# Kernel tuning notes

Hardware: AMD Instinct MI355X
Metric: run time of the kernel (lower is better)

Reference implementation:

```python
import jax, jax.numpy as jnp
import numpy as np

H = 1.0  # RBF bandwidth (init kwarg h)


def setup_inputs() -> dict:
    key = jax.random.key(0)
    k1, k2 = jax.random.split(key)
    x = jax.random.normal(k1, (8192, 512), dtype=jnp.float32)
    x1 = jax.random.normal(k2, (8192, 512), dtype=jnp.float32)
    return {"x": x, "x1": x1}


def reference(x, x1):
    # exp(-||x_i - x1_j||^2 / h), computed via the GEMM trick to avoid the
    # O(N*M*D) broadcast intermediate the original torch code materializes.
    x_sq = jnp.sum(x * x, axis=-1, keepdims=True)          # [N, 1]
    x1_sq = jnp.sum(x1 * x1, axis=-1)                       # [M]
    cross = jnp.einsum('nd,md->nm', x, x1)                  # [N, M]
    d = jnp.maximum(x_sq + x1_sq[None, :] - 2.0 * cross, 0.0)
    return jnp.exp(-d / H)
```

## Files before the change

### kernel.cpp

```cpp
#include <hip/hip_runtime.h>
#include <stdint.h>
#include <stddef.h>


#define NROWS 8192
#define DIMK  512
#define BM    128
#define BN    128
#define BK    32
#define KTILES (DIMK / BK)

typedef __bf16 bf16x8 __attribute__((ext_vector_type(8)));
typedef float  f32x4  __attribute__((ext_vector_type(4)));

#define AS1 __attribute__((address_space(1)))
#define AS3 __attribute__((address_space(3)))

__device__ __forceinline__ uint32_t f2bf(float f) {
    uint32_t u = __float_as_uint(f);
    return (u + 0x7FFFu + ((u >> 16) & 1u)) >> 16;
}

__global__ __launch_bounds__(256) void precast_full(
    const float* __restrict__ x, const float* __restrict__ x1,
    uint16_t* __restrict__ xb, uint16_t* __restrict__ x1b,
    float* __restrict__ xsq, float* __restrict__ x1sq)
{
    const int row = blockIdx.x;
    const float* src;
    uint16_t* dstb;
    float* dsts;
    if (blockIdx.y == 0) { src = x  + (size_t)row * DIMK; dstb = xb  + (size_t)row * DIMK; dsts = xsq  + row; }
    else                 { src = x1 + (size_t)row * DIMK; dstb = x1b + (size_t)row * DIMK; dsts = x1sq + row; }
    const int t = threadIdx.x;
    float2 v = ((const float2*)src)[t];
    float s = v.x * v.x + v.y * v.y;
    ((uint32_t*)dstb)[t] = f2bf(v.x) | (f2bf(v.y) << 16);
    #pragma unroll
    for (int off = 32; off > 0; off >>= 1) s += __shfl_down(s, off);
    __shared__ float red[4];
    if ((t & 63) == 0) red[t >> 6] = s;
    __syncthreads();
    if (t == 0) *dsts = red[0] + red[1] + red[2] + red[3];
}

__global__ __launch_bounds__(256) void norms_only(
    const float* __restrict__ x, const float* __restrict__ x1,
    float* __restrict__ xsq, float* __restrict__ x1sq)
{
    const int row = blockIdx.x;
    const float* src = (blockIdx.y == 0) ? x + (size_t)row * DIMK : x1 + (size_t)row * DIMK;
    float* dsts      = (blockIdx.y == 0) ? xsq + row : x1sq + row;
    const int t = threadIdx.x;
    float2 v = ((const float2*)src)[t];
    float s = v.x * v.x + v.y * v.y;
    #pragma unroll
    for (int off = 32; off > 0; off >>= 1) s += __shfl_down(s, off);
    __shared__ float red[4];
    if ((t & 63) == 0) red[t >> 6] = s;
    __syncthreads();
    if (t == 0) *dsts = red[0] + red[1] + red[2] + red[3];
}

__global__ __launch_bounds__(256) void rbf_mfma_pre(
    const uint16_t* __restrict__ Xb, const uint16_t* __restrict__ X1b,
    const float* __restrict__ xsq, const float* __restrict__ x1sq,
    float* __restrict__ out)
{
    __shared__ uint16_t As[BM * BK];
    __shared__ uint16_t Bs[BN * BK];

    const int t    = threadIdx.x;
    const int bm   = blockIdx.x;
    const int bn   = blockIdx.y;
    const int lane = t & 63;
    const int w    = t >> 6;
    const int wm   = w >> 1;
    const int wn   = w & 1;

    const int srow = t >> 2;
    const int scol = (t & 3) * 8;
    const uint16_t* gA = Xb  + (size_t)(bm * BM + srow) * DIMK + scol;
    const uint16_t* gB = X1b + (size_t)(bn * BN + srow) * DIMK + scol;
    uint16_t* lA = &As[t * 8];
    uint16_t* lB = &Bs[t * 8];

    f32x4 acc[4][4];
    #pragma unroll
    for (int i = 0; i < 4; ++i)
        #pragma unroll
        for (int j = 0; j < 4; ++j)
            acc[i][j] = f32x4{0.f, 0.f, 0.f, 0.f};

    const int lrow = lane & 15;
    const int kq   = (lane >> 4) * 8;
    int aoff[4], boff[4];
    #pragma unroll
    for (int i = 0; i < 4; ++i) {
        aoff[i] = (wm * 64 + i * 16 + lrow) * BK + kq;
        boff[i] = (wn * 64 + i * 16 + lrow) * BK + kq;
    }

    for (int kt = 0; kt < KTILES; ++kt) {
        const uint16_t* ga = gA + kt * BK;
        const uint16_t* gb = gB + kt * BK;
        __builtin_amdgcn_global_load_lds((AS1 void*)ga,               (AS3 void*)lA,          16, 0, 0);
        __builtin_amdgcn_global_load_lds((AS1 void*)(ga + 64 * DIMK), (AS3 void*)(lA + 2048), 16, 0, 0);
        __builtin_amdgcn_global_load_lds((AS1 void*)gb,               (AS3 void*)lB,          16, 0, 0);
        __builtin_amdgcn_global_load_lds((AS1 void*)(gb + 64 * DIMK), (AS3 void*)(lB + 2048), 16, 0, 0);
        __syncthreads();

        bf16x8 af[4], bg[4];
        #pragma unroll
        for (int i = 0; i < 4; ++i) af[i] = *(const bf16x8*)&As[aoff[i]];
        #pragma unroll
        for (int i = 0; i < 4; ++i) bg[i] = *(const bf16x8*)&Bs[boff[i]];
        #pragma unroll
        for (int i = 0; i < 4; ++i)
            #pragma unroll
            for (int j = 0; j < 4; ++j)
                acc[i][j] = __builtin_amdgcn_mfma_f32_16x16x32_bf16(af[i], bg[j], acc[i][j], 0, 0, 0);
        __syncthreads();
    }

    const int row0 = bm * BM + wm * 64 + (lane >> 4) * 4;
    const int col0 = bn * BN + wn * 64 + lrow;
    float xs[4][4], x1s[4];
    #pragma unroll
    for (int tm = 0; tm < 4; ++tm)
        #pragma unroll
        for (int r = 0; r < 4; ++r) xs[tm][r] = xsq[row0 + tm * 16 + r];
    #pragma unroll
    for (int tn = 0; tn < 4; ++tn) x1s[tn] = x1sq[col0 + tn * 16];

    #pragma unroll
    for (int tm = 0; tm < 4; ++tm)
        #pragma unroll
        for (int tn = 0; tn < 4; ++tn)
            #pragma unroll
            for (int r = 0; r < 4; ++r) {
                const int row = row0 + tm * 16 + r;
                const int col = col0 + tn * 16;
                float d = xs[tm][r] + x1s[tn] - 2.0f * acc[tm][tn][r];
                d = fmaxf(d, 0.0f);
                out[(size_t)row * NROWS + col] = __expf(-d);
            }
}

__global__ __launch_bounds__(256) void rbf_mfma_inline(
    const float* __restrict__ X, const float* __restrict__ X1,
    const float* __restrict__ xsq, const float* __restrict__ x1sq,
    float* __restrict__ out)
{
    __shared__ uint16_t As[BM * BK];
    __shared__ uint16_t Bs[BN * BK];

    const int t    = threadIdx.x;
    const int bm   = blockIdx.x;
    const int bn   = blockIdx.y;
    const int lane = t & 63;
    const int w    = t >> 6;
    const int wm   = w >> 1;
    const int wn   = w & 1;

    f32x4 acc[4][4];
    #pragma unroll
    for (int i = 0; i < 4; ++i)
        #pragma unroll
        for (int j = 0; j < 4; ++j)
            acc[i][j] = f32x4{0.f, 0.f, 0.f, 0.f};

    const int lrow = lane & 15;
    const int kq   = (lane >> 4) * 8;
    int aoff[4], boff[4];
    #pragma unroll
    for (int i = 0; i < 4; ++i) {
        aoff[i] = (wm * 64 + i * 16 + lrow) * BK + kq;
        boff[i] = (wn * 64 + i * 16 + lrow) * BK + kq;
    }

    for (int kt = 0; kt < KTILES; ++kt) {
        #pragma unroll
        for (int i = 0; i < 4; ++i) {
            const int g   = t + i * 256;
            const int row = g >> 3;
            const int c4  = (g & 7) * 4;
            float4 va = *(const float4*)&X [(size_t)(bm * BM + row) * DIMK + kt * BK + c4];
            float4 vb = *(const float4*)&X1[(size_t)(bn * BN + row) * DIMK + kt * BK + c4];
            uint2 pa, pb;
            pa.x = f2bf(va.x) | (f2bf(va.y) << 16);
            pa.y = f2bf(va.z) | (f2bf(va.w) << 16);
            pb.x = f2bf(vb.x) | (f2bf(vb.y) << 16);
            pb.y = f2bf(vb.z) | (f2bf(vb.w) << 16);
            *(uint2*)&As[g * 4] = pa;
            *(uint2*)&Bs[g * 4] = pb;
        }
        __syncthreads();

        bf16x8 af[4], bg[4];
        #pragma unroll
        for (int i = 0; i < 4; ++i) af[i] = *(const bf16x8*)&As[aoff[i]];
        #pragma unroll
        for (int i = 0; i < 4; ++i) bg[i] = *(const bf16x8*)&Bs[boff[i]];
        #pragma unroll
        for (int i = 0; i < 4; ++i)
            #pragma unroll
            for (int j = 0; j < 4; ++j)
                acc[i][j] = __builtin_amdgcn_mfma_f32_16x16x32_bf16(af[i], bg[j], acc[i][j], 0, 0, 0);
        __syncthreads();
    }

    const int row0 = bm * BM + wm * 64 + (lane >> 4) * 4;
    const int col0 = bn * BN + wn * 64 + lrow;
    float xs[4][4], x1s[4];
    #pragma unroll
    for (int tm = 0; tm < 4; ++tm)
        #pragma unroll
        for (int r = 0; r < 4; ++r) xs[tm][r] = xsq[row0 + tm * 16 + r];
    #pragma unroll
    for (int tn = 0; tn < 4; ++tn) x1s[tn] = x1sq[col0 + tn * 16];

    #pragma unroll
    for (int tm = 0; tm < 4; ++tm)
        #pragma unroll
        for (int tn = 0; tn < 4; ++tn)
            #pragma unroll
            for (int r = 0; r < 4; ++r) {
                const int row = row0 + tm * 16 + r;
                const int col = col0 + tn * 16;
                float d = xs[tm][r] + x1s[tn] - 2.0f * acc[tm][tn][r];
                d = fmaxf(d, 0.0f);
                out[(size_t)row * NROWS + col] = __expf(-d);
            }
}

extern "C" void kernel_launch(void* const* d_in, const int* in_sizes, int n_in,
                              void* d_out, int out_size, void* d_ws, size_t ws_size,
                              hipStream_t stream)
{
    const float* x  = (const float*)d_in[0];
    const float* x1 = (const float*)d_in[1];
    float* out = (float*)d_out;

    const size_t bf_bytes  = (size_t)NROWS * DIMK * sizeof(uint16_t);
    const size_t need_full = 2 * bf_bytes + 2 * (size_t)NROWS * sizeof(float);

    dim3 gridG(NROWS / BM, NROWS / BN);

    if (ws_size >= need_full) {
        uint16_t* xb   = (uint16_t*)d_ws;
        uint16_t* x1b  = xb + (size_t)NROWS * DIMK;
        float*    xsq  = (float*)((char*)d_ws + 2 * bf_bytes);
        float*    x1sq = xsq + NROWS;
        precast_full<<<dim3(NROWS, 2), 256, 0, stream>>>(x, x1, xb, x1b, xsq, x1sq);
        rbf_mfma_pre<<<gridG, 256, 0, stream>>>(xb, x1b, xsq, x1sq, out);
    } else {
        float* xsq  = (float*)d_ws;
        float* x1sq = xsq + NROWS;
        norms_only<<<dim3(NROWS, 2), 256, 0, stream>>>(x, x1, xsq, x1sq);
        rbf_mfma_inline<<<gridG, 256, 0, stream>>>(x, x1, xsq, x1sq, out);
    }
}
```

Measured before the change: 350.5 us.

## Quantize inputs to FP8 e4m3 and use scaled 16x16x128 MFMA

Replaces the bf16 pre-cast with an FP8 e4m3 pre-cast (one wave per row, no shared-memory reduction). The GEMM kernel now uses the mfma_scale 16x16x128 f8f6f4 instruction with unit scales and a K tile of 128. That gives four K iterations instead of sixteen and halves the operand bytes loaded per tile. The intent is to cut MFMA issue count, barriers and global traffic. The cost is much coarser precision in the cross term, which could hurt accuracy for inputs whose distances are small.

```diff
diff --git a/kernel.cpp b/kernel.cpp
--- a/kernel.cpp
+++ b/kernel.cpp
@@ -7,10 +7,11 @@
 #define DIMK  512
 #define BM    128
 #define BN    128
-#define BK    32
-#define KTILES (DIMK / BK)
+#define BKB   128
+#define KT    (DIMK / BKB)
 
 typedef __bf16 bf16x8 __attribute__((ext_vector_type(8)));
+typedef int    i32x8  __attribute__((ext_vector_type(8)));
 typedef float  f32x4  __attribute__((ext_vector_type(4)));
 
 #define AS1 __attribute__((address_space(1)))
@@ -21,27 +22,50 @@
     return (u + 0x7FFFu + ((u >> 16) & 1u)) >> 16;
 }
 
-__global__ __launch_bounds__(256) void precast_full(
+__device__ __forceinline__ uint32_t f2e4m3(float f) {
+    uint32_t u   = __float_as_uint(f);
+    uint32_t s   = (u >> 24) & 0x80u;
+    uint32_t abs = u & 0x7FFFFFFFu;
+    if (abs >= 0x43E00000u)
+        return s | 0x7Eu;
+    if (abs < 0x3C800000u) {
+        uint32_t m = (uint32_t)rintf(__uint_as_float(abs) * 512.0f);
+        return s | m;
+    }
+    uint32_t lsb = (abs >> 20) & 1u;
+    uint32_t r   = abs + 0x7FFFFu + lsb;
+    uint32_t e   = (r >> 23) - 127u + 7u;
+    uint32_t m   = (r >> 20) & 7u;
+    return s | (e << 3) | m;
+}
+
+__global__ __launch_bounds__(256) void precast_fp8(
     const float* __restrict__ x, const float* __restrict__ x1,
-    uint16_t* __restrict__ xb, uint16_t* __restrict__ x1b,
+    uint8_t* __restrict__ xf, uint8_t* __restrict__ x1f,
     float* __restrict__ xsq, float* __restrict__ x1sq)
 {
-    const int row = blockIdx.x;
+    const int w    = threadIdx.x >> 6;
+    const int lane = threadIdx.x & 63;
+    const int row  = blockIdx.x * 4 + w;
     const float* src;
-    uint16_t* dstb;
+    uint8_t* dstb;
     float* dsts;
-    if (blockIdx.y == 0) { src = x  + (size_t)row * DIMK; dstb = xb  + (size_t)row * DIMK; dsts = xsq  + row; }
-    else                 { src = x1 + (size_t)row * DIMK; dstb = x1b + (size_t)row * DIMK; dsts = x1sq + row; }
-    const int t = threadIdx.x;
-    float2 v = ((const float2*)src)[t];
-    float s = v.x * v.x + v.y * v.y;
-    ((uint32_t*)dstb)[t] = f2bf(v.x) | (f2bf(v.y) << 16);
+    if (blockIdx.y == 0) { src = x  + (size_t)row * DIMK; dstb = xf  + (size_t)row * DIMK; dsts = xsq  + row; }
+    else                 { src = x1 + (size_t)row * DIMK; dstb = x1f + (size_t)row * DIMK; dsts = x1sq + row; }
+
+    float4 v0 = ((const float4*)src)[lane * 2];
+    float4 v1 = ((const float4*)src)[lane * 2 + 1];
+    float s = v0.x * v0.x + v0.y * v0.y + v0.z * v0.z + v0.w * v0.w
+            + v1.x * v1.x + v1.y * v1.y + v1.z * v1.z + v1.w * v1.w;
+
+    uint2 p;
+    p.x = f2e4m3(v0.x) | (f2e4m3(v0.y) << 8) | (f2e4m3(v0.z) << 16) | (f2e4m3(v0.w) << 24);
+    p.y = f2e4m3(v1.x) | (f2e4m3(v1.y) << 8) | (f2e4m3(v1.z) << 16) | (f2e4m3(v1.w) << 24);
+    ((uint2*)dstb)[lane] = p;
+
     #pragma unroll
     for (int off = 32; off > 0; off >>= 1) s += __shfl_down(s, off);
-    __shared__ float red[4];
-    if ((t & 63) == 0) red[t >> 6] = s;
-    __syncthreads();
-    if (t == 0) *dsts = red[0] + red[1] + red[2] + red[3];
+    if (lane == 0) *dsts = s;
 }
 
 __global__ __launch_bounds__(256) void norms_only(
@@ -62,13 +86,13 @@
     if (t == 0) *dsts = red[0] + red[1] + red[2] + red[3];
 }
 
-__global__ __launch_bounds__(256) void rbf_mfma_pre(
-    const uint16_t* __restrict__ Xb, const uint16_t* __restrict__ X1b,
+__global__ __launch_bounds__(256) void rbf_mfma_mxfp8(
+    const uint8_t* __restrict__ Xf, const uint8_t* __restrict__ X1f,
     const float* __restrict__ xsq, const float* __restrict__ x1sq,
     float* __restrict__ out)
 {
-    __shared__ uint16_t As[BM * BK];
-    __shared__ uint16_t Bs[BN * BK];
+    __shared__ uint8_t As[BM * BKB];
+    __shared__ uint8_t Bs[BN * BKB];
 
     const int t    = threadIdx.x;
     const int bm   = blockIdx.x;
@@ -78,51 +102,14 @@
     const int wm   = w >> 1;
     const int wn   = w & 1;
 
-    const int srow = t >> 2;
-    const int scol = (t & 3) * 8;
-    const uint16_t* gA = Xb  + (size_t)(bm * BM + srow) * DIMK + scol;
-    const uint16_t* gB = X1b + (size_t)(bn * BN + srow) * DIMK + scol;
-    uint16_t* lA = &As[t * 8];
-    uint16_t* lB = &Bs[t * 8];
-
-    f32x4 acc[4][4];
-    #pragma unroll
-    for (int i = 0; i < 4; ++i)
-        #pragma unroll
-        for (int j = 0; j < 4; ++j)
-            acc[i][j] = f32x4{0.f, 0.f, 0.f, 0.f};
+    const int srow = t >> 3;
+    const int scol = (t & 7) * 16;
+    const uint8_t* gA = Xf  + (size_t)(bm * BM + srow) * DIMK + scol;
+    const uint8_t* gB = X1f + (size_t)(bn * BN + srow) * DIMK + scol;
+    uint8_t* lA = &As[t * 16];
+    uint8_t* lB = &Bs[t * 16];
 
     const int lrow = lane & 15;
-    const int kq   = (lane >> 4) * 8;
-    int aoff[4], boff[4];
-    #pragma unroll
-    for (int i = 0; i < 4; ++i) {
-        aoff[i] = (wm * 64 + i * 16 + lrow) * BK + kq;
-        boff[i] = (wn * 64 + i * 16 + lrow) * BK + kq;
-    }
-
-    for (int kt = 0; kt < KTILES; ++kt) {
-        const uint16_t* ga = gA + kt * BK;
-        const uint16_t* gb = gB + kt * BK;
-        __builtin_amdgcn_global_load_lds((AS1 void*)ga,               (AS3 void*)lA,          16, 0, 0);
-        __builtin_amdgcn_global_load_lds((AS1 void*)(ga + 64 * DIMK), (AS3 void*)(lA + 2048), 16, 0, 0);
-        __builtin_amdgcn_global_load_lds((AS1 void*)gb,               (AS3 void*)lB,          16, 0, 0);
-        __builtin_amdgcn_global_load_lds((AS1 void*)(gb + 64 * DIMK), (AS3 void*)(lB + 2048), 16, 0, 0);
-        __syncthreads();
-
-        bf16x8 af[4], bg[4];
-        #pragma unroll
-        for (int i = 0; i < 4; ++i) af[i] = *(const bf16x8*)&As[aoff[i]];
-        #pragma unroll
-        for (int i = 0; i < 4; ++i) bg[i] = *(const bf16x8*)&Bs[boff[i]];
-        #pragma unroll
-        for (int i = 0; i < 4; ++i)
-            #pragma unroll
-            for (int j = 0; j < 4; ++j)
-                acc[i][j] = __builtin_amdgcn_mfma_f32_16x16x32_bf16(af[i], bg[j], acc[i][j], 0, 0, 0);
-        __syncthreads();
-    }
-
     const int row0 = bm * BM + wm * 64 + (lane >> 4) * 4;
     const int col0 = bn * BN + wn * 64 + lrow;
     float xs[4][4], x1s[4];
@@ -132,6 +119,51 @@
         for (int r = 0; r < 4; ++r) xs[tm][r] = xsq[row0 + tm * 16 + r];
     #pragma unroll
     for (int tn = 0; tn < 4; ++tn) x1s[tn] = x1sq[col0 + tn * 16];
+
+    f32x4 acc[4][4];
+    #pragma unroll
+    for (int i = 0; i < 4; ++i)
+        #pragma unroll
+        for (int j = 0; j < 4; ++j)
+            acc[i][j] = f32x4{0.f, 0.f, 0.f, 0.f};
+
+    const int kq = (lane >> 4) * 32;
+    int aoff[4], boff[4];
+    #pragma unroll
+    for (int i = 0; i < 4; ++i) {
+        aoff[i] = (wm * 64 + i * 16 + lrow) * BKB + kq;
+        boff[i] = (wn * 64 + i * 16 + lrow) * BKB + kq;
+    }
+
+    #pragma unroll
+    for (int kt = 0; kt < KT; ++kt) {
+        const uint8_t* ga = gA + kt * BKB;
+        const uint8_t* gb = gB + kt * BKB;
+        #pragma unroll
+        for (int c = 0; c < 4; ++c) {
+            __builtin_amdgcn_global_load_lds((AS1 void*)(ga + (size_t)c * 32 * DIMK),
+                                             (AS3 void*)(lA + c * 4096), 16, 0, 0);
+            __builtin_amdgcn_global_load_lds((AS1 void*)(gb + (size_t)c * 32 * DIMK),
+                                             (AS3 void*)(lB + c * 4096), 16, 0, 0);
+        }
+        __syncthreads();
+
+        i32x8 af[4], bg[4];
+        #pragma unroll
+        for (int i = 0; i < 4; ++i) af[i] = *(const i32x8*)&As[aoff[i]];
+        #pragma unroll
+        for (int i = 0; i < 4; ++i) bg[i] = *(const i32x8*)&Bs[boff[i]];
+        #pragma unroll
+        for (int i = 0; i < 4; ++i)
+            #pragma unroll
+            for (int j = 0; j < 4; ++j)
+                acc[i][j] = __builtin_amdgcn_mfma_scale_f32_16x16x128_f8f6f4(
+                    af[i], bg[j], acc[i][j],
+                    0, 0,
+                    0, 0x7F7F7F7F,
+                    0, 0x7F7F7F7F);
+        __syncthreads();
+    }
 
     #pragma unroll
     for (int tm = 0; tm < 4; ++tm)
@@ -152,8 +184,8 @@
     const float* __restrict__ xsq, const float* __restrict__ x1sq,
     float* __restrict__ out)
 {
-    __shared__ uint16_t As[BM * BK];
-    __shared__ uint16_t Bs[BN * BK];
+    __shared__ uint16_t As[BM * 32];
+    __shared__ uint16_t Bs[BN * 32];
 
     const int t    = threadIdx.x;
     const int bm   = blockIdx.x;
@@ -175,18 +207,18 @@
     int aoff[4], boff[4];
     #pragma unroll
     for (int i = 0; i < 4; ++i) {
-        aoff[i] = (wm * 64 + i * 16 + lrow) * BK + kq;
-        boff[i] = (wn * 64 + i * 16 + lrow) * BK + kq;
-    }
-
-    for (int kt = 0; kt < KTILES; ++kt) {
+        aoff[i] = (wm * 64 + i * 16 + lrow) * 32 + kq;
+        boff[i] = (wn * 64 + i * 16 + lrow) * 32 + kq;
+    }
+
+    for (int kt = 0; kt < DIMK / 32; ++kt) {
         #pragma unroll
         for (int i = 0; i < 4; ++i) {
             const int g   = t + i * 256;
             const int row = g >> 3;
             const int c4  = (g & 7) * 4;
-            float4 va = *(const float4*)&X [(size_t)(bm * BM + row) * DIMK + kt * BK + c4];
-            float4 vb = *(const float4*)&X1[(size_t)(bn * BN + row) * DIMK + kt * BK + c4];
+            float4 va = *(const float4*)&X [(size_t)(bm * BM + row) * DIMK + kt * 32 + c4];
+            float4 vb = *(const float4*)&X1[(size_t)(bn * BN + row) * DIMK + kt * 32 + c4];
             uint2 pa, pb;
             pa.x = f2bf(va.x) | (f2bf(va.y) << 16);
             pa.y = f2bf(va.z) | (f2bf(va.w) << 16);
@@ -242,18 +274,18 @@
     const float* x1 = (const float*)d_in[1];
     float* out = (float*)d_out;
 
-    const size_t bf_bytes  = (size_t)NROWS * DIMK * sizeof(uint16_t);
-    const size_t need_full = 2 * bf_bytes + 2 * (size_t)NROWS * sizeof(float);
+    const size_t f8_bytes  = (size_t)NROWS * DIMK;
+    const size_t need_full = 2 * f8_bytes + 2 * (size_t)NROWS * sizeof(float);
 
     dim3 gridG(NROWS / BM, NROWS / BN);
 
     if (ws_size >= need_full) {
-        uint16_t* xb   = (uint16_t*)d_ws;
-        uint16_t* x1b  = xb + (size_t)NROWS * DIMK;
-        float*    xsq  = (float*)((char*)d_ws + 2 * bf_bytes);
-        float*    x1sq = xsq + NROWS;
-        precast_full<<<dim3(NROWS, 2), 256, 0, stream>>>(x, x1, xb, x1b, xsq, x1sq);
-        rbf_mfma_pre<<<gridG, 256, 0, stream>>>(xb, x1b, xsq, x1sq, out);
+        uint8_t* xf   = (uint8_t*)d_ws;
+        uint8_t* x1f  = xf + f8_bytes;
+        float*   xsq  = (float*)((char*)d_ws + 2 * f8_bytes);
+        float*   x1sq = xsq + NROWS;
+        precast_fp8<<<dim3(NROWS / 4, 2), 256, 0, stream>>>(x, x1, xf, x1f, xsq, x1sq);
+        rbf_mfma_mxfp8<<<gridG, 256, 0, stream>>>(xf, x1f, xsq, x1sq, out);
     } else {
         float* xsq  = (float*)d_ws;
         float* x1sq = xsq + NROWS;
```

Result: faster. 314.2 us (-10.4%).
